# Kernel optimization log

Hardware: AMD Instinct MI355X
Metric: run time of the kernel (lower is better)

## Reference

```python
import jax, jax.numpy as jnp
import numpy as np

ALPHA = 0.2        # LeakyReLU negative slope (self.alpha)
NEG = -9e15        # mask value used by the torch module


def gru_cell(x, h, W_ih, W_hh, b_ih, b_hh):
    """torch.nn.GRUCell math. x, h: [N, F]; W_*: [3F, F]; b_*: [3F]. Gate order r,z,n."""
    gi = x @ W_ih.T + b_ih
    gh = h @ W_hh.T + b_hh
    ir, iz, i_n = jnp.split(gi, 3, axis=-1)
    hr, hz, h_n = jnp.split(gh, 3, axis=-1)
    r = jax.nn.sigmoid(ir + hr)
    z = jax.nn.sigmoid(iz + hz)
    n = jnp.tanh(i_n + r * h_n)
    return (1.0 - z) * n + z * h


def setup_inputs() -> dict:
    key = jax.random.key(0)
    N, F = 8192, 256
    ks = jax.random.split(key, 8)
    inputs = jax.random.normal(ks[0], (N, F), jnp.float32)
    # GRUCell parameters
    W_ih = jax.random.normal(ks[1], (3 * F, F), jnp.float32) / np.sqrt(F)
    W_hh = jax.random.normal(ks[2], (3 * F, F), jnp.float32) / np.sqrt(F)
    b_ih = jax.random.normal(ks[3], (3 * F,), jnp.float32) * 0.01
    b_hh = jax.random.normal(ks[4], (3 * F,), jnp.float32) * 0.01
    # GAT attention vector a: [2F, 1]
    a = jax.random.normal(ks[5], (2 * F, 1), jnp.float32) / np.sqrt(2.0 * F)
    # per-node neighbor pair (encodes weight_dict's 1-/2-neighbor cases)
    nbr = jax.random.randint(ks[6], (N, 2), 0, N)
    # dense adjacency, values in {0,1}
    adj = jax.random.randint(ks[7], (N, N), 0, 2).astype(jnp.int32)
    return dict(inputs=inputs, W_ih=W_ih, W_hh=W_hh, b_ih=b_ih, b_hh=b_hh,
                a=a, nbr=nbr, adj=adj)


def reference(inputs, W_ih, W_hh, b_ih, b_hh, a, nbr, adj):
    F_dim = inputs.shape[1]
    # per-node GRU aggregation: hidden = neighbor1 feature, input = neighbor2 feature
    h = inputs[nbr[:, 0]]                      # [N, F]
    x = inputs[nbr[:, 1]]                      # [N, F]
    outs = gru_cell(x, h, W_ih, W_hh, b_ih, b_hh)  # [N, F]
    # GAT scores: e[i,j] = leakyrelu([outs_i || outs_j] . a) = leakyrelu(f1_i + f2_j)
    # (decomposed -- avoids materializing the [N*N, 2F] concat of the original)
    a1 = a[:F_dim, 0]                          # [F]
    a2 = a[F_dim:, 0]                          # [F]
    e = jax.nn.leaky_relu((outs @ a1)[:, None] + (outs @ a2)[None, :], ALPHA)  # [N, N]
    e = jnp.where(adj > 0, e, NEG)
    return jax.nn.softmax(e, axis=1)
```

## Files before the change

kernel.cpp:

```cpp
#include <hip/hip_runtime.h>
#include <hip/hip_bf16.h>

#define NN 8192
#define FF 256
#define NEGV -9000000000000000.0f

typedef __bf16 bf16x8 __attribute__((ext_vector_type(8)));
typedef float f32x4 __attribute__((ext_vector_type(4)));

__device__ __forceinline__ void load_lds16(const void* g, void* l) {
  auto gp = (const __attribute__((address_space(1))) void*)(uintptr_t)g;
  auto lp = (__attribute__((address_space(3))) void*)(uint32_t)(uintptr_t)l;
  __builtin_amdgcn_global_load_lds(gp, lp, 16, 0, 0);
}

__global__ __launch_bounds__(256) void k_gather_bf16(const float* __restrict__ inputs,
                                                     const int* __restrict__ nbr,
                                                     __hip_bfloat16* __restrict__ Abf) {
  const int gid = blockIdx.x * 256 + threadIdx.x;
  const int m = gid >> 6;
  const int c = (gid & 63) << 2;
  const int src = (m < NN) ? nbr[2 * m + 1] : nbr[2 * (m - NN)];
  const float4 v = *(const float4*)(inputs + (size_t)src * FF + c);
  union { __hip_bfloat16 h[4]; uint2 u; } t;
  t.h[0] = __float2bfloat16(v.x);
  t.h[1] = __float2bfloat16(v.y);
  t.h[2] = __float2bfloat16(v.z);
  t.h[3] = __float2bfloat16(v.w);
  *(uint2*)(Abf + (size_t)m * FF + c) = t.u;
}

__global__ __launch_bounds__(256) void k_conv_w(const float* __restrict__ Wih,
                                                const float* __restrict__ Whh,
                                                __hip_bfloat16* __restrict__ Bbf) {
  const int gid = blockIdx.x * 256 + threadIdx.x;
  const int r = gid >> 6;
  const int c = (gid & 63) << 2;
  const float* src = (r < 768) ? (Wih + (size_t)r * FF + c) : (Whh + (size_t)(r - 768) * FF + c);
  const float4 v = *(const float4*)src;
  union { __hip_bfloat16 h[4]; uint2 u; } t;
  t.h[0] = __float2bfloat16(v.x);
  t.h[1] = __float2bfloat16(v.y);
  t.h[2] = __float2bfloat16(v.z);
  t.h[3] = __float2bfloat16(v.w);
  *(uint2*)(Bbf + (size_t)r * FF + c) = t.u;
}

#define BM 128
#define BN 128
#define BK 64
__global__ __launch_bounds__(256) void k_gemm(const __hip_bfloat16* __restrict__ A,
                                              const __hip_bfloat16* __restrict__ B,
                                              float* __restrict__ C) {
  __shared__ __align__(16) __hip_bfloat16 As[BM * BK];
  __shared__ __align__(16) __hip_bfloat16 Bs[BN * BK];
  const int m0 = blockIdx.y * BM;
  const int n0t = blockIdx.x * BN;
  const int wbase = (m0 < NN) ? 0 : 768;
  const int n0 = n0t + wbase;
  const int tid = threadIdx.x;
  const int w = tid >> 6, l = tid & 63;
  const int wm = w >> 1, wn = w & 1;

  f32x4 acc[4][4] = {};

  for (int k0 = 0; k0 < FF; k0 += BK) {
#pragma unroll
    for (int c = 0; c < 4; ++c) {
      const int chunk = w * 4 + c;
      const int rrow = chunk * 8 + (l >> 3);
      const int kk = (l & 7) * 8;
      load_lds16(A + (size_t)(m0 + rrow) * FF + k0 + kk, (char*)As + chunk * 1024);
      load_lds16(B + (size_t)(n0 + rrow) * FF + k0 + kk, (char*)Bs + chunk * 1024);
    }
    __syncthreads();
#pragma unroll
    for (int kk = 0; kk < 2; ++kk) {
      bf16x8 af[4], bfr[4];
#pragma unroll
      for (int m = 0; m < 4; ++m) {
        const int row = wm * 64 + m * 16 + (l & 15);
        const int k = kk * 32 + (l >> 4) * 8;
        af[m] = *(const bf16x8*)&As[row * BK + k];
      }
#pragma unroll
      for (int n = 0; n < 4; ++n) {
        const int col = wn * 64 + n * 16 + (l & 15);
        const int k = kk * 32 + (l >> 4) * 8;
        bfr[n] = *(const bf16x8*)&Bs[col * BK + k];
      }
#pragma unroll
      for (int m = 0; m < 4; ++m)
#pragma unroll
        for (int n = 0; n < 4; ++n)
          acc[m][n] = __builtin_amdgcn_mfma_f32_16x16x32_bf16(af[m], bfr[n], acc[m][n], 0, 0, 0);
    }
    __syncthreads();
  }
#pragma unroll
  for (int m = 0; m < 4; ++m) {
#pragma unroll
    for (int n = 0; n < 4; ++n) {
      const int col = n0t + wn * 64 + n * 16 + (l & 15);
      const int rbase = m0 + wm * 64 + m * 16 + (l >> 4) * 4;
#pragma unroll
      for (int j = 0; j < 4; ++j)
        C[(size_t)(rbase + j) * 768 + col] = acc[m][n][j];
    }
  }
}

__global__ __launch_bounds__(256) void k_combine(const float* __restrict__ C,
                                                 const float* __restrict__ inputs,
                                                 const int* __restrict__ nbr,
                                                 const float* __restrict__ b_ih,
                                                 const float* __restrict__ b_hh,
                                                 const float* __restrict__ a,
                                                 float* __restrict__ s1,
                                                 float* __restrict__ s2) {
  const int i = blockIdx.x;
  const int c = threadIdx.x;
  const float* Ci = C + (size_t)i * 768;
  const float* Ch = C + (size_t)(NN + i) * 768;
  const float ir = Ci[c]       + b_ih[c];
  const float iz = Ci[256 + c] + b_ih[256 + c];
  const float in_ = Ci[512 + c] + b_ih[512 + c];
  const float hr = Ch[c]       + b_hh[c];
  const float hz = Ch[256 + c] + b_hh[256 + c];
  const float hn = Ch[512 + c] + b_hh[512 + c];
  const float r = 1.f / (1.f + __expf(-(ir + hr)));
  const float z = 1.f / (1.f + __expf(-(iz + hz)));
  const float n = tanhf(in_ + r * hn);
  const float h = inputs[(size_t)nbr[2 * i] * FF + c];
  const float o = (1.f - z) * n + z * h;
  float p1 = o * a[c];
  float p2 = o * a[256 + c];
#pragma unroll
  for (int off = 32; off; off >>= 1) {
    p1 += __shfl_xor(p1, off);
    p2 += __shfl_xor(p2, off);
  }
  __shared__ float w1[4], w2[4];
  if ((c & 63) == 0) { w1[c >> 6] = p1; w2[c >> 6] = p2; }
  __syncthreads();
  if (c == 0) {
    s1[i] = w1[0] + w1[1] + w1[2] + w1[3];
    s2[i] = w2[0] + w2[1] + w2[2] + w2[3];
  }
}

__global__ __launch_bounds__(256) void k_softmax(const int* __restrict__ adj,
                                                 const float* __restrict__ s1,
                                                 const float* __restrict__ s2,
                                                 float* __restrict__ out) {
  __shared__ __align__(16) float s2s[NN];
  __shared__ float red[8];
  const int row = blockIdx.x;
  const int t = threadIdx.x;
#pragma unroll
  for (int k = 0; k < 8; ++k) {
    const int v = k * 256 + t;
    *(float4*)(s2s + v * 4) = *(const float4*)(s2 + v * 4);
  }
  const float s1v = s1[row];
  __syncthreads();
  const int4* adjv = (const int4*)(adj + (size_t)row * NN);
  float e[32];
  float tmax = -3.4e38f;
#pragma unroll
  for (int k = 0; k < 8; ++k) {
    const int v = k * 256 + t;
    const int4 a4 = adjv[v];
    const float4 sv = *(const float4*)(s2s + v * 4);
    float x0 = s1v + sv.x; x0 = (x0 > 0.f) ? x0 : 0.2f * x0;
    float x1 = s1v + sv.y; x1 = (x1 > 0.f) ? x1 : 0.2f * x1;
    float x2 = s1v + sv.z; x2 = (x2 > 0.f) ? x2 : 0.2f * x2;
    float x3 = s1v + sv.w; x3 = (x3 > 0.f) ? x3 : 0.2f * x3;
    e[4 * k + 0] = (a4.x > 0) ? x0 : NEGV;
    e[4 * k + 1] = (a4.y > 0) ? x1 : NEGV;
    e[4 * k + 2] = (a4.z > 0) ? x2 : NEGV;
    e[4 * k + 3] = (a4.w > 0) ? x3 : NEGV;
    tmax = fmaxf(tmax, fmaxf(fmaxf(e[4 * k], e[4 * k + 1]), fmaxf(e[4 * k + 2], e[4 * k + 3])));
  }
#pragma unroll
  for (int off = 32; off; off >>= 1) tmax = fmaxf(tmax, __shfl_xor(tmax, off));
  if ((t & 63) == 0) red[t >> 6] = tmax;
  __syncthreads();
  const float rmax = fmaxf(fmaxf(red[0], red[1]), fmaxf(red[2], red[3]));
  float tsum = 0.f;
#pragma unroll
  for (int i = 0; i < 32; ++i) { e[i] = __expf(e[i] - rmax); tsum += e[i]; }
#pragma unroll
  for (int off = 32; off; off >>= 1) tsum += __shfl_xor(tsum, off);
  if ((t & 63) == 0) red[4 + (t >> 6)] = tsum;
  __syncthreads();
  const float inv = 1.f / (red[4] + red[5] + red[6] + red[7]);
  float* orow = out + (size_t)row * NN;
#pragma unroll
  for (int k = 0; k < 8; ++k) {
    const int v = k * 256 + t;
    float4 o;
    o.x = e[4 * k + 0] * inv;
    o.y = e[4 * k + 1] * inv;
    o.z = e[4 * k + 2] * inv;
    o.w = e[4 * k + 3] * inv;
    *(float4*)(orow + v * 4) = o;
  }
}

extern "C" void kernel_launch(void* const* d_in, const int* in_sizes, int n_in,
                              void* d_out, int out_size, void* d_ws, size_t ws_size,
                              hipStream_t stream) {
  const float* inputs = (const float*)d_in[0];
  const float* W_ih   = (const float*)d_in[1];
  const float* W_hh   = (const float*)d_in[2];
  const float* b_ih   = (const float*)d_in[3];
  const float* b_hh   = (const float*)d_in[4];
  const float* a      = (const float*)d_in[5];
  const int*   nbr    = (const int*)d_in[6];
  const int*   adj    = (const int*)d_in[7];
  float* out = (float*)d_out;

  float* Cbuf = out;
  __hip_bfloat16* Abf = (__hip_bfloat16*)((char*)d_out + (64u << 20));
  __hip_bfloat16* Bbf = (__hip_bfloat16*)((char*)d_out + (80u << 20));
  float* s1 = (float*)d_ws;
  float* s2 = s1 + NN;

  k_gather_bf16<<<4096, 256, 0, stream>>>(inputs, nbr, Abf);
  k_conv_w<<<384, 256, 0, stream>>>(W_ih, W_hh, Bbf);
  k_gemm<<<dim3(6, 128), 256, 0, stream>>>(Abf, Bbf, Cbuf);
  k_combine<<<NN, 256, 0, stream>>>(Cbuf, inputs, nbr, b_ih, b_hh, a, s1, s2);
  k_softmax<<<NN, 256, 0, stream>>>(adj, s1, s2, out);
}
```

Measured before the change: 137.7 us.

## Fuse GRU GEMM with gate epilogue and GAT score reduction in one kernel

Replaces the gather, weight-convert, GEMM and combine kernels with a single conversion kernel and a fused GRU kernel. The fused kernel gathers neighbor rows straight into swizzled LDS, runs MFMA against weights read from global memory, and applies the gate math plus the a1/a2 dot products in registers. This removes the fp32 C intermediate round trip and two launches. In exchange it uses only 256 blocks and reads the B operand directly from global/L2 with no LDS reuse, which may limit occupancy and bandwidth.

```diff
diff --git a/kernel.cpp b/kernel.cpp
--- a/kernel.cpp
+++ b/kernel.cpp
@@ -14,138 +14,165 @@
   __builtin_amdgcn_global_load_lds(gp, lp, 16, 0, 0);
 }
 
-__global__ __launch_bounds__(256) void k_gather_bf16(const float* __restrict__ inputs,
-                                                     const int* __restrict__ nbr,
-                                                     __hip_bfloat16* __restrict__ Abf) {
+__global__ __launch_bounds__(256) void k_convert(const float* __restrict__ inputs,
+                                                 const float* __restrict__ Wih,
+                                                 const float* __restrict__ Whh,
+                                                 __hip_bfloat16* __restrict__ ibf,
+                                                 __hip_bfloat16* __restrict__ Wc) {
   const int gid = blockIdx.x * 256 + threadIdx.x;
-  const int m = gid >> 6;
-  const int c = (gid & 63) << 2;
-  const int src = (m < NN) ? nbr[2 * m + 1] : nbr[2 * (m - NN)];
-  const float4 v = *(const float4*)(inputs + (size_t)src * FF + c);
-  union { __hip_bfloat16 h[4]; uint2 u; } t;
-  t.h[0] = __float2bfloat16(v.x);
-  t.h[1] = __float2bfloat16(v.y);
-  t.h[2] = __float2bfloat16(v.z);
-  t.h[3] = __float2bfloat16(v.w);
-  *(uint2*)(Abf + (size_t)m * FF + c) = t.u;
-}
-
-__global__ __launch_bounds__(256) void k_conv_w(const float* __restrict__ Wih,
-                                                const float* __restrict__ Whh,
-                                                __hip_bfloat16* __restrict__ Bbf) {
-  const int gid = blockIdx.x * 256 + threadIdx.x;
-  const int r = gid >> 6;
-  const int c = (gid & 63) << 2;
-  const float* src = (r < 768) ? (Wih + (size_t)r * FF + c) : (Whh + (size_t)(r - 768) * FF + c);
-  const float4 v = *(const float4*)src;
-  union { __hip_bfloat16 h[4]; uint2 u; } t;
-  t.h[0] = __float2bfloat16(v.x);
-  t.h[1] = __float2bfloat16(v.y);
-  t.h[2] = __float2bfloat16(v.z);
-  t.h[3] = __float2bfloat16(v.w);
-  *(uint2*)(Bbf + (size_t)r * FF + c) = t.u;
-}
-
-#define BM 128
-#define BN 128
-#define BK 64
-__global__ __launch_bounds__(256) void k_gemm(const __hip_bfloat16* __restrict__ A,
-                                              const __hip_bfloat16* __restrict__ B,
-                                              float* __restrict__ C) {
-  __shared__ __align__(16) __hip_bfloat16 As[BM * BK];
-  __shared__ __align__(16) __hip_bfloat16 Bs[BN * BK];
-  const int m0 = blockIdx.y * BM;
-  const int n0t = blockIdx.x * BN;
-  const int wbase = (m0 < NN) ? 0 : 768;
-  const int n0 = n0t + wbase;
+  const size_t NI = (size_t)NN * FF;
+  const size_t base = (size_t)gid * 8;
+  const float* src;
+  __hip_bfloat16* dst;
+  if (base < NI) { src = inputs + base; dst = ibf + base; }
+  else {
+    const size_t wo = base - NI;
+    dst = Wc + wo;
+    src = (wo < 196608) ? (Wih + wo) : (Whh + (wo - 196608));
+  }
+  const float4 v0 = *(const float4*)src;
+  const float4 v1 = *(const float4*)(src + 4);
+  union { __hip_bfloat16 h[8]; uint4 u; } t;
+  t.h[0] = __float2bfloat16(v0.x); t.h[1] = __float2bfloat16(v0.y);
+  t.h[2] = __float2bfloat16(v0.z); t.h[3] = __float2bfloat16(v0.w);
+  t.h[4] = __float2bfloat16(v1.x); t.h[5] = __float2bfloat16(v1.y);
+  t.h[6] = __float2bfloat16(v1.z); t.h[7] = __float2bfloat16(v1.w);
+  *(uint4*)dst = t.u;
+}
+
+__global__ __launch_bounds__(256) void k_gru(const __hip_bfloat16* __restrict__ ibf,
+                                             const __hip_bfloat16* __restrict__ Wc,
+                                             const float* __restrict__ inputs,
+                                             const int* __restrict__ nbr,
+                                             const float* __restrict__ b_ih,
+                                             const float* __restrict__ b_hh,
+                                             const float* __restrict__ a,
+                                             float* __restrict__ s1,
+                                             float* __restrict__ s2) {
+  __shared__ __align__(16) __hip_bfloat16 Ax[32 * 256];
+  __shared__ __align__(16) __hip_bfloat16 Ah[32 * 256];
+  __shared__ int hrow_s[32];
+  __shared__ float r1[4][32], r2[4][32];
+  const int rb = blockIdx.x * 32;
   const int tid = threadIdx.x;
   const int w = tid >> 6, l = tid & 63;
-  const int wm = w >> 1, wn = w & 1;
-
-  f32x4 acc[4][4] = {};
-
-  for (int k0 = 0; k0 < FF; k0 += BK) {
-#pragma unroll
-    for (int c = 0; c < 4; ++c) {
-      const int chunk = w * 4 + c;
-      const int rrow = chunk * 8 + (l >> 3);
-      const int kk = (l & 7) * 8;
-      load_lds16(A + (size_t)(m0 + rrow) * FF + k0 + kk, (char*)As + chunk * 1024);
-      load_lds16(B + (size_t)(n0 + rrow) * FF + k0 + kk, (char*)Bs + chunk * 1024);
-    }
-    __syncthreads();
-#pragma unroll
-    for (int kk = 0; kk < 2; ++kk) {
-      bf16x8 af[4], bfr[4];
-#pragma unroll
-      for (int m = 0; m < 4; ++m) {
-        const int row = wm * 64 + m * 16 + (l & 15);
-        const int k = kk * 32 + (l >> 4) * 8;
-        af[m] = *(const bf16x8*)&As[row * BK + k];
-      }
-#pragma unroll
-      for (int n = 0; n < 4; ++n) {
-        const int col = wn * 64 + n * 16 + (l & 15);
-        const int k = kk * 32 + (l >> 4) * 8;
-        bfr[n] = *(const bf16x8*)&Bs[col * BK + k];
-      }
-#pragma unroll
-      for (int m = 0; m < 4; ++m)
-#pragma unroll
-        for (int n = 0; n < 4; ++n)
-          acc[m][n] = __builtin_amdgcn_mfma_f32_16x16x32_bf16(af[m], bfr[n], acc[m][n], 0, 0, 0);
-    }
-    __syncthreads();
-  }
-#pragma unroll
-  for (int m = 0; m < 4; ++m) {
-#pragma unroll
-    for (int n = 0; n < 4; ++n) {
-      const int col = n0t + wn * 64 + n * 16 + (l & 15);
-      const int rbase = m0 + wm * 64 + m * 16 + (l >> 4) * 4;
-#pragma unroll
-      for (int j = 0; j < 4; ++j)
-        C[(size_t)(rbase + j) * 768 + col] = acc[m][n][j];
-    }
-  }
-}
-
-__global__ __launch_bounds__(256) void k_combine(const float* __restrict__ C,
-                                                 const float* __restrict__ inputs,
-                                                 const int* __restrict__ nbr,
-                                                 const float* __restrict__ b_ih,
-                                                 const float* __restrict__ b_hh,
-                                                 const float* __restrict__ a,
-                                                 float* __restrict__ s1,
-                                                 float* __restrict__ s2) {
-  const int i = blockIdx.x;
-  const int c = threadIdx.x;
-  const float* Ci = C + (size_t)i * 768;
-  const float* Ch = C + (size_t)(NN + i) * 768;
-  const float ir = Ci[c]       + b_ih[c];
-  const float iz = Ci[256 + c] + b_ih[256 + c];
-  const float in_ = Ci[512 + c] + b_ih[512 + c];
-  const float hr = Ch[c]       + b_hh[c];
-  const float hz = Ch[256 + c] + b_hh[256 + c];
-  const float hn = Ch[512 + c] + b_hh[512 + c];
-  const float r = 1.f / (1.f + __expf(-(ir + hr)));
-  const float z = 1.f / (1.f + __expf(-(iz + hz)));
-  const float n = tanhf(in_ + r * hn);
-  const float h = inputs[(size_t)nbr[2 * i] * FF + c];
-  const float o = (1.f - z) * n + z * h;
-  float p1 = o * a[c];
-  float p2 = o * a[256 + c];
-#pragma unroll
-  for (int off = 32; off; off >>= 1) {
-    p1 += __shfl_xor(p1, off);
-    p2 += __shfl_xor(p2, off);
-  }
-  __shared__ float w1[4], w2[4];
-  if ((c & 63) == 0) { w1[c >> 6] = p1; w2[c >> 6] = p2; }
-  __syncthreads();
-  if (c == 0) {
-    s1[i] = w1[0] + w1[1] + w1[2] + w1[3];
-    s2[i] = w2[0] + w2[1] + w2[2] + w2[3];
+  const int fl = l & 15, q = l >> 4;
+
+  if (tid < 32) hrow_s[tid] = nbr[2 * (rb + tid)];
+
+  {
+    const int rlb = w * 8;
+#pragma unroll
+    for (int j = 0; j < 4; ++j) {
+      const int r = rlb + j * 2 + (l >> 5);
+      const int cs = l & 31;
+      const int gc = cs ^ (r & 7);
+      const int xr = nbr[2 * (rb + r) + 1];
+      const int hr_ = nbr[2 * (rb + r)];
+      load_lds16((const char*)(ibf + (size_t)xr * FF) + gc * 16,
+                 (char*)Ax + (rlb + j * 2) * 512);
+      load_lds16((const char*)(ibf + (size_t)hr_ * FF) + gc * 16,
+                 (char*)Ah + (rlb + j * 2) * 512);
+    }
+  }
+  __syncthreads();
+
+  float p1[8] = {0.f, 0.f, 0.f, 0.f, 0.f, 0.f, 0.f, 0.f};
+  float p2[8] = {0.f, 0.f, 0.f, 0.f, 0.f, 0.f, 0.f, 0.f};
+
+  for (int fb = 0; fb < 4; ++fb) {
+    const int f = fb * 64 + w * 16 + fl;
+    const float bir = b_ih[f], biz = b_ih[256 + f], bin_ = b_ih[512 + f];
+    const float bhr = b_hh[f], bhz = b_hh[256 + f], bhn = b_hh[512 + f];
+    const float a1f = a[f], a2f = a[256 + f];
+
+    f32x4 acc[6][2];
+#pragma unroll
+    for (int g = 0; g < 6; ++g) { acc[g][0] = (f32x4){0,0,0,0}; acc[g][1] = (f32x4){0,0,0,0}; }
+
+    bf16x8 af[2][8];
+#pragma unroll
+    for (int m = 0; m < 2; ++m)
+#pragma unroll
+      for (int ks = 0; ks < 8; ++ks) {
+        const int row = m * 16 + fl;
+        const int c = ks * 4 + q;
+        af[m][ks] = *(const bf16x8*)((const char*)Ax + row * 512 + (c ^ (row & 7)) * 16);
+      }
+#pragma unroll
+    for (int g = 0; g < 3; ++g) {
+      const __hip_bfloat16* bp = Wc + (size_t)(g * 256 + f) * FF + q * 8;
+#pragma unroll
+      for (int ks = 0; ks < 8; ++ks) {
+        const bf16x8 bf = *(const bf16x8*)(bp + ks * 32);
+        acc[g][0] = __builtin_amdgcn_mfma_f32_16x16x32_bf16(af[0][ks], bf, acc[g][0], 0, 0, 0);
+        acc[g][1] = __builtin_amdgcn_mfma_f32_16x16x32_bf16(af[1][ks], bf, acc[g][1], 0, 0, 0);
+      }
+    }
+#pragma unroll
+    for (int m = 0; m < 2; ++m)
+#pragma unroll
+      for (int ks = 0; ks < 8; ++ks) {
+        const int row = m * 16 + fl;
+        const int c = ks * 4 + q;
+        af[m][ks] = *(const bf16x8*)((const char*)Ah + row * 512 + (c ^ (row & 7)) * 16);
+      }
+#pragma unroll
+    for (int g = 0; g < 3; ++g) {
+      const __hip_bfloat16* bp = Wc + (size_t)(768 + g * 256 + f) * FF + q * 8;
+#pragma unroll
+      for (int ks = 0; ks < 8; ++ks) {
+        const bf16x8 bf = *(const bf16x8*)(bp + ks * 32);
+        acc[3 + g][0] = __builtin_amdgcn_mfma_f32_16x16x32_bf16(af[0][ks], bf, acc[3 + g][0], 0, 0, 0);
+        acc[3 + g][1] = __builtin_amdgcn_mfma_f32_16x16x32_bf16(af[1][ks], bf, acc[3 + g][1], 0, 0, 0);
+      }
+    }
+
+#pragma unroll
+    for (int m = 0; m < 2; ++m)
+#pragma unroll
+      for (int j = 0; j < 4; ++j) {
+        const int row = m * 16 + q * 4 + j;
+        const float ir = acc[0][m][j] + bir;
+        const float iz = acc[1][m][j] + biz;
+        const float in_ = acc[2][m][j] + bin_;
+        const float hrv = acc[3][m][j] + bhr;
+        const float hzv = acc[4][m][j] + bhz;
+        const float hnv = acc[5][m][j] + bhn;
+        const float r_ = 1.f / (1.f + __expf(-(ir + hrv)));
+        const float z_ = 1.f / (1.f + __expf(-(iz + hzv)));
+        const float n_ = tanhf(in_ + r_ * hnv);
+        const float hval = inputs[(size_t)hrow_s[row] * FF + f];
+        const float o = (1.f - z_) * n_ + z_ * hval;
+        p1[m * 4 + j] += o * a1f;
+        p2[m * 4 + j] += o * a2f;
+      }
+  }
+
+#pragma unroll
+  for (int i = 0; i < 8; ++i) {
+#pragma unroll
+    for (int off = 1; off < 16; off <<= 1) {
+      p1[i] += __shfl_xor(p1[i], off);
+      p2[i] += __shfl_xor(p2[i], off);
+    }
+  }
+  if (fl == 0) {
+#pragma unroll
+    for (int m = 0; m < 2; ++m)
+#pragma unroll
+      for (int j = 0; j < 4; ++j) {
+        const int row = m * 16 + q * 4 + j;
+        r1[w][row] = p1[m * 4 + j];
+        r2[w][row] = p2[m * 4 + j];
+      }
+  }
+  __syncthreads();
+  if (tid < 32) {
+    s1[rb + tid] = r1[0][tid] + r1[1][tid] + r1[2][tid] + r1[3][tid];
+  } else if (tid < 64) {
+    const int t2 = tid - 32;
+    s2[rb + t2] = r2[0][t2] + r2[1][t2] + r2[2][t2] + r2[3][t2];
   }
 }
 
@@ -221,15 +248,12 @@
   const int*   adj    = (const int*)d_in[7];
   float* out = (float*)d_out;
 
-  float* Cbuf = out;
-  __hip_bfloat16* Abf = (__hip_bfloat16*)((char*)d_out + (64u << 20));
-  __hip_bfloat16* Bbf = (__hip_bfloat16*)((char*)d_out + (80u << 20));
+  __hip_bfloat16* ibf = (__hip_bfloat16*)((char*)d_out + (64u << 20));
+  __hip_bfloat16* Wc  = (__hip_bfloat16*)((char*)d_out + (80u << 20));
   float* s1 = (float*)d_ws;
   float* s2 = s1 + NN;
 
-  k_gather_bf16<<<4096, 256, 0, stream>>>(inputs, nbr, Abf);
-  k_conv_w<<<384, 256, 0, stream>>>(W_ih, W_hh, Bbf);
-  k_gemm<<<dim3(6, 128), 256, 0, stream>>>(Abf, Bbf, Cbuf);
-  k_combine<<<NN, 256, 0, stream>>>(Cbuf, inputs, nbr, b_ih, b_hh, a, s1, s2);
+  k_convert<<<1216, 256, 0, stream>>>(inputs, W_ih, W_hh, ibf, Wc);
+  k_gru<<<256, 256, 0, stream>>>(ibf, Wc, inputs, nbr, b_ih, b_hh, a, s1, s2);
   k_softmax<<<NN, 256, 0, stream>>>(adj, s1, s2, out);
 }
```

Measured after the change: 156.1 us. +13.3%, slower.
